# Optimization experiments

Measured on AMD Instinct MI355X. Metric: run time of the kernel, lower is better.

Reference implementation:

```python
import jax, jax.numpy as jnp
import numpy as np

EPS = 1e-6

def _rms_norm(x, w):
    # normalize over last dim (head_dim)
    var = jnp.mean(jnp.square(x), axis=-1, keepdims=True)
    return x * jax.lax.rsqrt(var + EPS) * w

def _rotate_half(x):
    half = x.shape[-1] // 2
    first, second = x[..., :half], x[..., half:]
    return jnp.concatenate([-second, first], axis=-1)

def _apply_rope(x, cos, sin):
    # x: [B,H,S,D]; cos/sin: [B,S,D] -> broadcast over heads
    return x * cos[:, None] + _rotate_half(x) * sin[:, None]

def setup_inputs() -> dict:
    key = jax.random.key(0)
    ks = jax.random.split(key, 10)
    B, Sq, Sk, Dm, H = 2, 2048, 2048, 2048, 16
    hd = Dm // H
    scale = 1.0 / np.sqrt(Dm)
    return {
        "x": jax.random.normal(ks[0], (B, Sq, Dm), jnp.float32),
        "context": jax.random.normal(ks[1], (B, Sk, Dm), jnp.float32),
        "cos_q": jax.random.uniform(ks[2], (B, Sq, hd), jnp.float32),
        "sin_q": jax.random.uniform(ks[3], (B, Sq, hd), jnp.float32),
        "cos_k": jax.random.uniform(ks[4], (B, Sk, hd), jnp.float32),
        "sin_k": jax.random.uniform(ks[5], (B, Sk, hd), jnp.float32),
        "Wq": jax.random.normal(ks[6], (Dm, Dm), jnp.float32) * scale,
        "Wk": jax.random.normal(ks[7], (Dm, Dm), jnp.float32) * scale,
        "Wv": jax.random.normal(ks[8], (Dm, Dm), jnp.float32) * scale,
        "Wo": jax.random.normal(ks[9], (Dm, Dm), jnp.float32) * scale,
        "q_norm_w": jnp.ones((hd,), jnp.float32),
        "k_norm_w": jnp.ones((hd,), jnp.float32),
    }

def reference(x, context, cos_q, sin_q, cos_k, sin_k, Wq, Wk, Wv, Wo, q_norm_w, k_norm_w):
    B, Sq, Dm = x.shape
    hd = q_norm_w.shape[0]
    H = Dm // hd
    # projections (torch Linear: y = x @ W.T), reshape to [B,H,S,D]
    q = (x @ Wq.T).reshape(B, Sq, H, hd).transpose(0, 2, 1, 3)
    k = (context @ Wk.T).reshape(B, -1, H, hd).transpose(0, 2, 1, 3)
    v = (context @ Wv.T).reshape(B, -1, H, hd).transpose(0, 2, 1, 3)
    # per-head QK RMSNorm
    q = _rms_norm(q, q_norm_w)
    k = _rms_norm(k, k_norm_w)
    # RoPE
    q = _apply_rope(q, cos_q, sin_q)
    k = _apply_rope(k, cos_k, sin_k)
    # SDPA, scale = 1/sqrt(head_dim)
    scale = 1.0 / np.sqrt(hd).astype(np.float32)
    scores = jnp.einsum('bhqd,bhkd->bhqk', q, k) * scale
    attn = jax.nn.softmax(scores, axis=-1)
    y = jnp.einsum('bhqk,bhkd->bhqd', attn, v)
    y = y.transpose(0, 2, 1, 3).reshape(B, Sq, Dm)
    return y @ Wo.T
```

## Files before the change

### kernel.cpp

```cpp
#include <hip/hip_runtime.h>


typedef __attribute__((ext_vector_type(8))) short bf16x8;
typedef __attribute__((ext_vector_type(4))) float f32x4;

#define AS1(p) ((__attribute__((address_space(1))) void*)(p))
#define AS3(p) ((__attribute__((address_space(3))) void*)(p))

__device__ __forceinline__ unsigned short f2bf(float f) {
  unsigned int u = __float_as_uint(f);
  u += 0x7fffu + ((u >> 16) & 1u);
  return (unsigned short)(u >> 16);
}

constexpr int B_ = 2, S_ = 2048, DM = 2048, H_ = 16, HD = 128;
constexpr int M_ = B_ * S_;

__global__ __launch_bounds__(256) void castbf(const float* __restrict__ X,
                                              unsigned short* __restrict__ Y, int n4) {
  int i = blockIdx.x * 256 + threadIdx.x;
  if (i >= n4) return;
  float4 v = ((const float4*)X)[i];
  ushort4 u;
  u.x = f2bf(v.x); u.y = f2bf(v.y); u.z = f2bf(v.z); u.w = f2bf(v.w);
  ((ushort4*)Y)[i] = u;
}

__global__ __launch_bounds__(256) void gemm_bt(const unsigned short* __restrict__ A,
                                               const unsigned short* __restrict__ Bw,
                                               float* __restrict__ C,
                                               int M, int N, int K) {
  __shared__ unsigned short lA[128 * 32];
  __shared__ unsigned short lB[128 * 32];
  const int tid = threadIdx.x, wave = tid >> 6, lane = tid & 63;
  const int quad = lane >> 4, l16 = lane & 15;
  const int m0 = blockIdx.x * 128, n0 = blockIdx.y * 128;
  const int wm = (wave >> 1) * 64, wn = (wave & 1) * 64;
  f32x4 acc[4][4];
#pragma unroll
  for (int i = 0; i < 4; i++)
#pragma unroll
    for (int j = 0; j < 4; j++) acc[i][j] = (f32x4){0.f, 0.f, 0.f, 0.f};

  for (int k0 = 0; k0 < K; k0 += 32) {
    __syncthreads();
#pragma unroll
    for (int call = 0; call < 2; ++call) {
      int c = wave * 128 + call * 64 + lane;
      int row = c >> 2, s = c & 3;
      int dc = s ^ ((row >> 1) & 3);
      __builtin_amdgcn_global_load_lds(AS1(A + (size_t)(m0 + row) * K + k0 + dc * 8),
                                       AS3(lA + (wave * 128 + call * 64) * 8), 16, 0, 0);
      __builtin_amdgcn_global_load_lds(AS1(Bw + (size_t)(n0 + row) * K + k0 + dc * 8),
                                       AS3(lB + (wave * 128 + call * 64) * 8), 16, 0, 0);
    }
    __syncthreads();

    bf16x8 af[4], bfr[4];
#pragma unroll
    for (int i = 0; i < 4; i++) {
      int r = wm + i * 16 + l16;
      af[i] = *(const bf16x8*)(lA + r * 32 + (quad ^ ((r >> 1) & 3)) * 8);
      int cN = wn + i * 16 + l16;
      bfr[i] = *(const bf16x8*)(lB + cN * 32 + (quad ^ ((cN >> 1) & 3)) * 8);
    }
#pragma unroll
    for (int i = 0; i < 4; i++)
#pragma unroll
      for (int j = 0; j < 4; j++)
        acc[i][j] = __builtin_amdgcn_mfma_f32_16x16x32_bf16(af[i], bfr[j], acc[i][j], 0, 0, 0);
  }
#pragma unroll
  for (int i = 0; i < 4; i++)
#pragma unroll
    for (int j = 0; j < 4; j++) {
      float* cp = C + (size_t)(m0 + wm + i * 16 + quad * 4) * N + (n0 + wn + j * 16 + l16);
#pragma unroll
      for (int r = 0; r < 4; r++) cp[(size_t)r * N] = acc[i][j][r];
    }
}

__global__ __launch_bounds__(256) void normrope(const float* __restrict__ X,
                                                const float* __restrict__ Cs,
                                                const float* __restrict__ Sn,
                                                const float* __restrict__ W,
                                                unsigned short* __restrict__ Out,
                                                float scale) {
  int gw = (blockIdx.x * 256 + threadIdx.x) >> 6;
  int lane = threadIdx.x & 63;
  int h = gw & 15, bs = gw >> 4;
  int s = bs & (S_ - 1), b = bs >> 11;
  const float* xr = X + (size_t)gw * HD;
  float x0 = xr[lane], x1 = xr[lane + 64];
  float ss = x0 * x0 + x1 * x1;
#pragma unroll
  for (int off = 32; off > 0; off >>= 1) ss += __shfl_xor(ss, off);
  float rr = rsqrtf(ss * (1.0f / 128.0f) + 1e-6f);
  float n0 = x0 * rr * W[lane], n1 = x1 * rr * W[lane + 64];
  const float* cp = Cs + (size_t)bs * HD;
  const float* sp = Sn + (size_t)bs * HD;
  float o0 = (n0 * cp[lane] - n1 * sp[lane]) * scale;
  float o1 = (n1 * cp[lane + 64] + n0 * sp[lane + 64]) * scale;
  unsigned short* orow = Out + (((size_t)(b * H_ + h)) * S_ + s) * HD;
  orow[lane] = f2bf(o0);
  orow[lane + 64] = f2bf(o1);
}

__global__ __launch_bounds__(256) void vtrans(const float* __restrict__ Vf,
                                              unsigned short* __restrict__ Vt) {
  __shared__ unsigned short tile[128 * 72];
  const int tid = threadIdx.x;
  const int sc = blockIdx.x & 31;
  const int bh = blockIdx.x >> 5;
  const int b = bh >> 4, h = bh & 15;
  const int s0 = sc * 64;
#pragma unroll
  for (int it = 0; it < 8; ++it) {
    int ci = it * 256 + tid;
    int s = ci >> 5, dq = ci & 31;
    float4 v = *(const float4*)(Vf + ((size_t)(b * S_ + s0 + s)) * DM + h * HD + dq * 4);
    unsigned short* tp = tile + (dq * 4) * 72 + s;
    tp[0] = f2bf(v.x); tp[72] = f2bf(v.y); tp[144] = f2bf(v.z); tp[216] = f2bf(v.w);
  }
  __syncthreads();
#pragma unroll
  for (int it = 0; it < 4; ++it) {
    int cj = it * 256 + tid;
    int d = cj >> 3, scx = cj & 7;
    bf16x8 vv = *(const bf16x8*)(tile + d * 72 + scx * 8);
    *(bf16x8*)(Vt + ((size_t)bh * HD + d) * S_ + s0 + scx * 8) = vv;
  }
}

__global__ __launch_bounds__(256) void flash(const unsigned short* __restrict__ Q,
                                             const unsigned short* __restrict__ Kt,
                                             const unsigned short* __restrict__ Vt,
                                             unsigned short* __restrict__ Y) {
  __shared__ unsigned short lK[32 * HD];
  __shared__ unsigned short lV[HD * 32];
  __shared__ unsigned short lP[4 * 32 * 32];
  const int tid = threadIdx.x, wave = tid >> 6, lane = tid & 63;
  const int quad = lane >> 4, l16 = lane & 15;
  const int qb = blockIdx.x & 15;
  const int bh = blockIdx.x >> 4;
  const int b = bh >> 4, h = bh & 15;
  const int q0 = qb * 128 + wave * 32;

  bf16x8 aq[2][4];
#pragma unroll
  for (int u = 0; u < 2; u++) {
    const unsigned short* qrow = Q + ((size_t)bh * S_ + q0 + u * 16 + l16) * HD;
#pragma unroll
    for (int t = 0; t < 4; t++) aq[u][t] = *(const bf16x8*)(qrow + t * 32 + quad * 8);
  }
  f32x4 o[2][8];
#pragma unroll
  for (int u = 0; u < 2; u++)
#pragma unroll
    for (int t = 0; t < 8; t++) o[u][t] = (f32x4){0.f, 0.f, 0.f, 0.f};
  float lsum[2][4] = {{0.f, 0.f, 0.f, 0.f}, {0.f, 0.f, 0.f, 0.f}};

  const unsigned short* kbase = Kt + (size_t)bh * S_ * HD;
  const unsigned short* vbase = Vt + (size_t)bh * HD * S_;
  unsigned short* lPw = lP + wave * 1024;
  const int mrow = quad * 4;
  const int xsl = (l16 >> 1) & 3;

  for (int k0 = 0; k0 < S_; k0 += 32) {
    __syncthreads();
#pragma unroll
    for (int call = 0; call < 2; ++call) {
      int c = wave * 128 + call * 64 + lane;
      int key = c >> 4, sk = c & 15;
      int dck = sk ^ (key & 15);
      __builtin_amdgcn_global_load_lds(AS1(kbase + (size_t)(k0 + key) * HD + dck * 8),
                                       AS3(lK + (wave * 128 + call * 64) * 8), 16, 0, 0);
      int dv = c >> 2, sv = c & 3;
      int kc = sv ^ ((dv >> 1) & 3);
      __builtin_amdgcn_global_load_lds(AS1(vbase + (size_t)dv * S_ + k0 + kc * 8),
                                       AS3(lV + (wave * 128 + call * 64) * 8), 16, 0, 0);
    }
    __syncthreads();

    f32x4 s0[2] = {(f32x4){0.f, 0.f, 0.f, 0.f}, (f32x4){0.f, 0.f, 0.f, 0.f}};
    f32x4 s1[2] = {(f32x4){0.f, 0.f, 0.f, 0.f}, (f32x4){0.f, 0.f, 0.f, 0.f}};
    {
      const unsigned short* krow0 = lK + l16 * HD;
      const unsigned short* krow1 = lK + (16 + l16) * HD;
#pragma unroll
      for (int t = 0; t < 4; t++) {
        int dcq = t * 4 + quad;
        bf16x8 kf0 = *(const bf16x8*)(krow0 + (dcq ^ l16) * 8);
        bf16x8 kf1 = *(const bf16x8*)(krow1 + (dcq ^ l16) * 8);
#pragma unroll
        for (int u = 0; u < 2; u++) {
          s0[u] = __builtin_amdgcn_mfma_f32_16x16x32_bf16(aq[u][t], kf0, s0[u], 0, 0, 0);
          s1[u] = __builtin_amdgcn_mfma_f32_16x16x32_bf16(aq[u][t], kf1, s1[u], 0, 0, 0);
        }
      }
    }
#pragma unroll
    for (int u = 0; u < 2; u++) {
      unsigned short* lPu = lPw + u * 512;
#pragma unroll
      for (int r = 0; r < 4; r++) {
        int m = mrow + r;
        int sx = (m >> 1) & 3;
        float p0 = __expf(s0[u][r]);
        float p1 = __expf(s1[u][r]);
        lsum[u][r] += p0 + p1;
        int kc0 = l16 >> 3;
        lPu[m * 32 + ((kc0 ^ sx)) * 8 + (l16 & 7)] = f2bf(p0);
        lPu[m * 32 + (((kc0 + 2) ^ sx)) * 8 + (l16 & 7)] = f2bf(p1);
      }
    }
    bf16x8 pf[2];
#pragma unroll
    for (int u = 0; u < 2; u++)
      pf[u] = *(const bf16x8*)(lPw + u * 512 + l16 * 32 + (quad ^ xsl) * 8);
#pragma unroll
    for (int t = 0; t < 8; t++) {
      bf16x8 vf = *(const bf16x8*)(lV + (t * 16 + l16) * 32 + (quad ^ xsl) * 8);
#pragma unroll
      for (int u = 0; u < 2; u++)
        o[u][t] = __builtin_amdgcn_mfma_f32_16x16x32_bf16(pf[u], vf, o[u][t], 0, 0, 0);
    }
  }

#pragma unroll
  for (int off = 1; off < 16; off <<= 1) {
#pragma unroll
    for (int u = 0; u < 2; u++)
#pragma unroll
      for (int r = 0; r < 4; r++) lsum[u][r] += __shfl_xor(lsum[u][r], off);
  }
  float inv[2][4];
#pragma unroll
  for (int u = 0; u < 2; u++)
#pragma unroll
    for (int r = 0; r < 4; r++) inv[u][r] = 1.0f / lsum[u][r];
#pragma unroll
  for (int u = 0; u < 2; u++)
#pragma unroll
    for (int t = 0; t < 8; t++)
#pragma unroll
      for (int r = 0; r < 4; r++) {
        size_t idx = ((size_t)b * S_ + q0 + u * 16 + mrow + r) * DM + h * HD + t * 16 + l16;
        Y[idx] = f2bf(o[u][t][r] * inv[u][r]);
      }
}

extern "C" void kernel_launch(void* const* d_in, const int* in_sizes, int n_in,
                              void* d_out, int out_size, void* d_ws, size_t ws_size,
                              hipStream_t stream) {
  const float* x    = (const float*)d_in[0];
  const float* ctx  = (const float*)d_in[1];
  const float* cosq = (const float*)d_in[2];
  const float* sinq = (const float*)d_in[3];
  const float* cosk = (const float*)d_in[4];
  const float* sink = (const float*)d_in[5];
  const float* Wq   = (const float*)d_in[6];
  const float* Wk   = (const float*)d_in[7];
  const float* Wv   = (const float*)d_in[8];
  const float* Wo   = (const float*)d_in[9];
  const float* qw   = (const float*)d_in[10];
  const float* kw   = (const float*)d_in[11];

  char* ws = (char*)d_ws;
  const size_t ACT2 = (size_t)M_ * DM * 2;
  const size_t W2   = (size_t)DM * DM * 2;
  unsigned short* xb  = (unsigned short*)(ws);
  unsigned short* cb  = (unsigned short*)(ws + ACT2);
  unsigned short* Wqb = (unsigned short*)(ws + 2 * ACT2);
  unsigned short* Wkb = (unsigned short*)(ws + 2 * ACT2 + W2);
  unsigned short* Wvb = (unsigned short*)(ws + 2 * ACT2 + 2 * W2);
  unsigned short* Wob = (unsigned short*)(ws + 2 * ACT2 + 3 * W2);
  float*          Pf  = (float*)(ws + 2 * ACT2 + 4 * W2);
  unsigned short* qn = xb;
  unsigned short* kn = Wqb;
  unsigned short* vt = cb;
  unsigned short* yb = (unsigned short*)Pf;

  const float scale = 0.0883883476483184f;
  dim3 gg(M_ / 128, DM / 128);

  castbf<<<M_ * DM / 1024, 256, 0, stream>>>(x, xb, M_ * DM / 4);
  castbf<<<M_ * DM / 1024, 256, 0, stream>>>(ctx, cb, M_ * DM / 4);
  castbf<<<DM * DM / 1024, 256, 0, stream>>>(Wq, Wqb, DM * DM / 4);
  castbf<<<DM * DM / 1024, 256, 0, stream>>>(Wk, Wkb, DM * DM / 4);
  castbf<<<DM * DM / 1024, 256, 0, stream>>>(Wv, Wvb, DM * DM / 4);
  castbf<<<DM * DM / 1024, 256, 0, stream>>>(Wo, Wob, DM * DM / 4);

  gemm_bt<<<gg, 256, 0, stream>>>(xb, Wqb, Pf, M_, DM, DM);
  normrope<<<M_ * H_ / 4, 256, 0, stream>>>(Pf, cosq, sinq, qw, qn, scale);

  gemm_bt<<<gg, 256, 0, stream>>>(cb, Wkb, Pf, M_, DM, DM);
  normrope<<<M_ * H_ / 4, 256, 0, stream>>>(Pf, cosk, sink, kw, kn, 1.0f);

  gemm_bt<<<gg, 256, 0, stream>>>(cb, Wvb, Pf, M_, DM, DM);
  vtrans<<<B_ * H_ * (S_ / 64), 256, 0, stream>>>(Pf, vt);

  flash<<<B_ * H_ * (S_ / 128), 256, 0, stream>>>(qn, kn, vt, yb);

  gemm_bt<<<gg, 256, 0, stream>>>(yb, Wob, (float*)d_out, M_, DM, DM);

  (void)in_sizes; (void)n_in; (void)out_size; (void)ws_size;
}
```

Baseline: 561.6 us.

## Batch QKV GEMMs into one launch with bf16 outputs; retile flash attention

The three projection GEMMs become a single launch with grid z selecting Q, K or V, and they write bf16 instead of fp32. That halves the intermediate traffic and removes the launch serialization between them. normrope and vtrans now read bf16 inputs. The flash kernel moves to 128-thread blocks covering 64 queries, with 64-key K/V tiles per sync, so there are twice as many blocks and half as many barriers per key. Rounding the projections to bf16 before the RMSNorm adds precision loss. The workspace now needs room for three separate projection buffers.

New measurement: 496.1 us. -11.7%, faster.

```diff
diff --git a/kernel.cpp b/kernel.cpp
--- a/kernel.cpp
+++ b/kernel.cpp
@@ -11,6 +11,9 @@
   unsigned int u = __float_as_uint(f);
   u += 0x7fffu + ((u >> 16) & 1u);
   return (unsigned short)(u >> 16);
+}
+__device__ __forceinline__ float bf2f(unsigned short u) {
+  return __uint_as_float(((unsigned int)u) << 16);
 }
 
 constexpr int B_ = 2, S_ = 2048, DM = 2048, H_ = 16, HD = 128;
@@ -24,6 +27,68 @@
   ushort4 u;
   u.x = f2bf(v.x); u.y = f2bf(v.y); u.z = f2bf(v.z); u.w = f2bf(v.w);
   ((ushort4*)Y)[i] = u;
+}
+
+__global__ __launch_bounds__(256) void gemm_qkv(const unsigned short* __restrict__ xb,
+                                                const unsigned short* __restrict__ cb,
+                                                const unsigned short* __restrict__ Wq,
+                                                const unsigned short* __restrict__ Wk,
+                                                const unsigned short* __restrict__ Wv,
+                                                unsigned short* __restrict__ Pq,
+                                                unsigned short* __restrict__ Pk,
+                                                unsigned short* __restrict__ Pv) {
+  __shared__ unsigned short lA[128 * 32];
+  __shared__ unsigned short lB[128 * 32];
+  const int z = blockIdx.z;
+  const unsigned short* A  = (z == 0) ? xb : cb;
+  const unsigned short* Bw = (z == 0) ? Wq : (z == 1) ? Wk : Wv;
+  unsigned short* C        = (z == 0) ? Pq : (z == 1) ? Pk : Pv;
+  const int tid = threadIdx.x, wave = tid >> 6, lane = tid & 63;
+  const int quad = lane >> 4, l16 = lane & 15;
+  const int m0 = blockIdx.x * 128, n0 = blockIdx.y * 128;
+  const int wm = (wave >> 1) * 64, wn = (wave & 1) * 64;
+  f32x4 acc[4][4];
+#pragma unroll
+  for (int i = 0; i < 4; i++)
+#pragma unroll
+    for (int j = 0; j < 4; j++) acc[i][j] = (f32x4){0.f, 0.f, 0.f, 0.f};
+
+  for (int k0 = 0; k0 < DM; k0 += 32) {
+    __syncthreads();
+#pragma unroll
+    for (int call = 0; call < 2; ++call) {
+      int c = wave * 128 + call * 64 + lane;
+      int row = c >> 2, s = c & 3;
+      int dc = s ^ ((row >> 1) & 3);
+      __builtin_amdgcn_global_load_lds(AS1(A + (size_t)(m0 + row) * DM + k0 + dc * 8),
+                                       AS3(lA + (wave * 128 + call * 64) * 8), 16, 0, 0);
+      __builtin_amdgcn_global_load_lds(AS1(Bw + (size_t)(n0 + row) * DM + k0 + dc * 8),
+                                       AS3(lB + (wave * 128 + call * 64) * 8), 16, 0, 0);
+    }
+    __syncthreads();
+
+    bf16x8 af[4], bfr[4];
+#pragma unroll
+    for (int i = 0; i < 4; i++) {
+      int r = wm + i * 16 + l16;
+      af[i] = *(const bf16x8*)(lA + r * 32 + (quad ^ ((r >> 1) & 3)) * 8);
+      int cN = wn + i * 16 + l16;
+      bfr[i] = *(const bf16x8*)(lB + cN * 32 + (quad ^ ((cN >> 1) & 3)) * 8);
+    }
+#pragma unroll
+    for (int i = 0; i < 4; i++)
+#pragma unroll
+      for (int j = 0; j < 4; j++)
+        acc[i][j] = __builtin_amdgcn_mfma_f32_16x16x32_bf16(af[i], bfr[j], acc[i][j], 0, 0, 0);
+  }
+#pragma unroll
+  for (int i = 0; i < 4; i++)
+#pragma unroll
+    for (int j = 0; j < 4; j++) {
+      unsigned short* cp = C + (size_t)(m0 + wm + i * 16 + quad * 4) * DM + (n0 + wn + j * 16 + l16);
+#pragma unroll
+      for (int r = 0; r < 4; r++) cp[(size_t)r * DM] = f2bf(acc[i][j][r]);
+    }
 }
 
 __global__ __launch_bounds__(256) void gemm_bt(const unsigned short* __restrict__ A,
@@ -80,7 +145,7 @@
     }
 }
 
-__global__ __launch_bounds__(256) void normrope(const float* __restrict__ X,
+__global__ __launch_bounds__(256) void normrope(const unsigned short* __restrict__ X,
                                                 const float* __restrict__ Cs,
                                                 const float* __restrict__ Sn,
                                                 const float* __restrict__ W,
@@ -90,8 +155,8 @@
   int lane = threadIdx.x & 63;
   int h = gw & 15, bs = gw >> 4;
   int s = bs & (S_ - 1), b = bs >> 11;
-  const float* xr = X + (size_t)gw * HD;
-  float x0 = xr[lane], x1 = xr[lane + 64];
+  const unsigned short* xr = X + (size_t)gw * HD;
+  float x0 = bf2f(xr[lane]), x1 = bf2f(xr[lane + 64]);
   float ss = x0 * x0 + x1 * x1;
 #pragma unroll
   for (int off = 32; off > 0; off >>= 1) ss += __shfl_xor(ss, off);
@@ -106,7 +171,7 @@
   orow[lane + 64] = f2bf(o1);
 }
 
-__global__ __launch_bounds__(256) void vtrans(const float* __restrict__ Vf,
+__global__ __launch_bounds__(256) void vtrans(const unsigned short* __restrict__ Vf,
                                               unsigned short* __restrict__ Vt) {
   __shared__ unsigned short tile[128 * 72];
   const int tid = threadIdx.x;
@@ -115,12 +180,13 @@
   const int b = bh >> 4, h = bh & 15;
   const int s0 = sc * 64;
 #pragma unroll
-  for (int it = 0; it < 8; ++it) {
+  for (int it = 0; it < 4; ++it) {
     int ci = it * 256 + tid;
-    int s = ci >> 5, dq = ci & 31;
-    float4 v = *(const float4*)(Vf + ((size_t)(b * S_ + s0 + s)) * DM + h * HD + dq * 4);
-    unsigned short* tp = tile + (dq * 4) * 72 + s;
-    tp[0] = f2bf(v.x); tp[72] = f2bf(v.y); tp[144] = f2bf(v.z); tp[216] = f2bf(v.w);
+    int s = ci >> 4, dc = ci & 15;
+    bf16x8 v = *(const bf16x8*)(Vf + ((size_t)(b * S_ + s0 + s)) * DM + h * HD + dc * 8);
+    unsigned short* tp = tile + (dc * 8) * 72 + s;
+#pragma unroll
+    for (int e = 0; e < 8; e++) tp[e * 72] = (unsigned short)v[e];
   }
   __syncthreads();
 #pragma unroll
@@ -132,19 +198,19 @@
   }
 }
 
-__global__ __launch_bounds__(256) void flash(const unsigned short* __restrict__ Q,
+__global__ __launch_bounds__(128) void flash(const unsigned short* __restrict__ Q,
                                              const unsigned short* __restrict__ Kt,
                                              const unsigned short* __restrict__ Vt,
                                              unsigned short* __restrict__ Y) {
-  __shared__ unsigned short lK[32 * HD];
-  __shared__ unsigned short lV[HD * 32];
-  __shared__ unsigned short lP[4 * 32 * 32];
+  __shared__ unsigned short lK[64 * HD];
+  __shared__ unsigned short lV[HD * 64];
+  __shared__ unsigned short lP[2 * 1024];
   const int tid = threadIdx.x, wave = tid >> 6, lane = tid & 63;
   const int quad = lane >> 4, l16 = lane & 15;
-  const int qb = blockIdx.x & 15;
-  const int bh = blockIdx.x >> 4;
+  const int qb = blockIdx.x & 31;
+  const int bh = blockIdx.x >> 5;
   const int b = bh >> 4, h = bh & 15;
-  const int q0 = qb * 128 + wave * 32;
+  const int q0 = qb * 64 + wave * 32;
 
   bf16x8 aq[2][4];
 #pragma unroll
@@ -165,65 +231,69 @@
   unsigned short* lPw = lP + wave * 1024;
   const int mrow = quad * 4;
   const int xsl = (l16 >> 1) & 3;
-
-  for (int k0 = 0; k0 < S_; k0 += 32) {
-    __syncthreads();
-#pragma unroll
-    for (int call = 0; call < 2; ++call) {
-      int c = wave * 128 + call * 64 + lane;
+  const int xsl7 = (l16 >> 1) & 7;
+
+  for (int k0 = 0; k0 < S_; k0 += 64) {
+    __syncthreads();
+#pragma unroll
+    for (int call = 0; call < 8; ++call) {
+      int c = call * 128 + wave * 64 + lane;
       int key = c >> 4, sk = c & 15;
       int dck = sk ^ (key & 15);
       __builtin_amdgcn_global_load_lds(AS1(kbase + (size_t)(k0 + key) * HD + dck * 8),
-                                       AS3(lK + (wave * 128 + call * 64) * 8), 16, 0, 0);
-      int dv = c >> 2, sv = c & 3;
-      int kc = sv ^ ((dv >> 1) & 3);
+                                       AS3(lK + (call * 128 + wave * 64) * 8), 16, 0, 0);
+      int dv = c >> 3, sv = c & 7;
+      int kc = sv ^ ((dv >> 1) & 7);
       __builtin_amdgcn_global_load_lds(AS1(vbase + (size_t)dv * S_ + k0 + kc * 8),
-                                       AS3(lV + (wave * 128 + call * 64) * 8), 16, 0, 0);
-    }
-    __syncthreads();
-
-    f32x4 s0[2] = {(f32x4){0.f, 0.f, 0.f, 0.f}, (f32x4){0.f, 0.f, 0.f, 0.f}};
-    f32x4 s1[2] = {(f32x4){0.f, 0.f, 0.f, 0.f}, (f32x4){0.f, 0.f, 0.f, 0.f}};
-    {
-      const unsigned short* krow0 = lK + l16 * HD;
-      const unsigned short* krow1 = lK + (16 + l16) * HD;
-#pragma unroll
-      for (int t = 0; t < 4; t++) {
-        int dcq = t * 4 + quad;
-        bf16x8 kf0 = *(const bf16x8*)(krow0 + (dcq ^ l16) * 8);
-        bf16x8 kf1 = *(const bf16x8*)(krow1 + (dcq ^ l16) * 8);
-#pragma unroll
-        for (int u = 0; u < 2; u++) {
-          s0[u] = __builtin_amdgcn_mfma_f32_16x16x32_bf16(aq[u][t], kf0, s0[u], 0, 0, 0);
-          s1[u] = __builtin_amdgcn_mfma_f32_16x16x32_bf16(aq[u][t], kf1, s1[u], 0, 0, 0);
+                                       AS3(lV + (call * 128 + wave * 64) * 8), 16, 0, 0);
+    }
+    __syncthreads();
+
+#pragma unroll
+    for (int h2 = 0; h2 < 2; ++h2) {
+      f32x4 s0[2] = {(f32x4){0.f, 0.f, 0.f, 0.f}, (f32x4){0.f, 0.f, 0.f, 0.f}};
+      f32x4 s1[2] = {(f32x4){0.f, 0.f, 0.f, 0.f}, (f32x4){0.f, 0.f, 0.f, 0.f}};
+      {
+        const unsigned short* krow0 = lK + (h2 * 32 + l16) * HD;
+        const unsigned short* krow1 = krow0 + 16 * HD;
+#pragma unroll
+        for (int t = 0; t < 4; t++) {
+          int dcq = t * 4 + quad;
+          bf16x8 kf0 = *(const bf16x8*)(krow0 + (dcq ^ l16) * 8);
+          bf16x8 kf1 = *(const bf16x8*)(krow1 + (dcq ^ l16) * 8);
+#pragma unroll
+          for (int u = 0; u < 2; u++) {
+            s0[u] = __builtin_amdgcn_mfma_f32_16x16x32_bf16(aq[u][t], kf0, s0[u], 0, 0, 0);
+            s1[u] = __builtin_amdgcn_mfma_f32_16x16x32_bf16(aq[u][t], kf1, s1[u], 0, 0, 0);
+          }
         }
       }
-    }
-#pragma unroll
-    for (int u = 0; u < 2; u++) {
-      unsigned short* lPu = lPw + u * 512;
-#pragma unroll
-      for (int r = 0; r < 4; r++) {
-        int m = mrow + r;
-        int sx = (m >> 1) & 3;
-        float p0 = __expf(s0[u][r]);
-        float p1 = __expf(s1[u][r]);
-        lsum[u][r] += p0 + p1;
-        int kc0 = l16 >> 3;
-        lPu[m * 32 + ((kc0 ^ sx)) * 8 + (l16 & 7)] = f2bf(p0);
-        lPu[m * 32 + (((kc0 + 2) ^ sx)) * 8 + (l16 & 7)] = f2bf(p1);
+#pragma unroll
+      for (int u = 0; u < 2; u++) {
+        unsigned short* lPu = lPw + u * 512;
+#pragma unroll
+        for (int r = 0; r < 4; r++) {
+          int m = mrow + r;
+          int sx = (m >> 1) & 3;
+          float p0 = __expf(s0[u][r]);
+          float p1 = __expf(s1[u][r]);
+          lsum[u][r] += p0 + p1;
+          int kc0 = l16 >> 3;
+          lPu[m * 32 + ((kc0 ^ sx)) * 8 + (l16 & 7)] = f2bf(p0);
+          lPu[m * 32 + (((kc0 + 2) ^ sx)) * 8 + (l16 & 7)] = f2bf(p1);
+        }
       }
-    }
-    bf16x8 pf[2];
-#pragma unroll
-    for (int u = 0; u < 2; u++)
-      pf[u] = *(const bf16x8*)(lPw + u * 512 + l16 * 32 + (quad ^ xsl) * 8);
-#pragma unroll
-    for (int t = 0; t < 8; t++) {
-      bf16x8 vf = *(const bf16x8*)(lV + (t * 16 + l16) * 32 + (quad ^ xsl) * 8);
+      bf16x8 pf[2];
 #pragma unroll
       for (int u = 0; u < 2; u++)
-        o[u][t] = __builtin_amdgcn_mfma_f32_16x16x32_bf16(pf[u], vf, o[u][t], 0, 0, 0);
+        pf[u] = *(const bf16x8*)(lPw + u * 512 + l16 * 32 + (quad ^ xsl) * 8);
+#pragma unroll
+      for (int t = 0; t < 8; t++) {
+        bf16x8 vf = *(const bf16x8*)(lV + (t * 16 + l16) * 64 + ((h2 * 4 + quad) ^ xsl7) * 8);
+#pragma unroll
+        for (int u = 0; u < 2; u++)
+          o[u][t] = __builtin_amdgcn_mfma_f32_16x16x32_bf16(pf[u], vf, o[u][t], 0, 0, 0);
+      }
     }
   }
 
@@ -275,14 +345,15 @@
   unsigned short* Wkb = (unsigned short*)(ws + 2 * ACT2 + W2);
   unsigned short* Wvb = (unsigned short*)(ws + 2 * ACT2 + 2 * W2);
   unsigned short* Wob = (unsigned short*)(ws + 2 * ACT2 + 3 * W2);
-  float*          Pf  = (float*)(ws + 2 * ACT2 + 4 * W2);
+  unsigned short* Pq  = (unsigned short*)(ws + 2 * ACT2 + 4 * W2);
+  unsigned short* Pk  = (unsigned short*)(ws + 3 * ACT2 + 4 * W2);
+  unsigned short* Pv  = (unsigned short*)(ws + 4 * ACT2 + 4 * W2);
   unsigned short* qn = xb;
   unsigned short* kn = Wqb;
   unsigned short* vt = cb;
-  unsigned short* yb = (unsigned short*)Pf;
+  unsigned short* yb = Pq;
 
   const float scale = 0.0883883476483184f;
-  dim3 gg(M_ / 128, DM / 128);
 
   castbf<<<M_ * DM / 1024, 256, 0, stream>>>(x, xb, M_ * DM / 4);
   castbf<<<M_ * DM / 1024, 256, 0, stream>>>(ctx, cb, M_ * DM / 4);
@@ -291,17 +362,16 @@
   castbf<<<DM * DM / 1024, 256, 0, stream>>>(Wv, Wvb, DM * DM / 4);
   castbf<<<DM * DM / 1024, 256, 0, stream>>>(Wo, Wob, DM * DM / 4);
 
-  gemm_bt<<<gg, 256, 0, stream>>>(xb, Wqb, Pf, M_, DM, DM);
-  normrope<<<M_ * H_ / 4, 256, 0, stream>>>(Pf, cosq, sinq, qw, qn, scale);
-
-  gemm_bt<<<gg, 256, 0, stream>>>(cb, Wkb, Pf, M_, DM, DM);
-  normrope<<<M_ * H_ / 4, 256, 0, stream>>>(Pf, cosk, sink, kw, kn, 1.0f);
-
-  gemm_bt<<<gg, 256, 0, stream>>>(cb, Wvb, Pf, M_, DM, DM);
-  vtrans<<<B_ * H_ * (S_ / 64), 256, 0, stream>>>(Pf, vt);
-
-  flash<<<B_ * H_ * (S_ / 128), 256, 0, stream>>>(qn, kn, vt, yb);
-
+  dim3 gq(M_ / 128, DM / 128, 3);
+  gemm_qkv<<<gq, 256, 0, stream>>>(xb, cb, Wqb, Wkb, Wvb, Pq, Pk, Pv);
+
+  normrope<<<M_ * H_ / 4, 256, 0, stream>>>(Pq, cosq, sinq, qw, qn, scale);
+  normrope<<<M_ * H_ / 4, 256, 0, stream>>>(Pk, cosk, sink, kw, kn, 1.0f);
+  vtrans<<<B_ * H_ * (S_ / 64), 256, 0, stream>>>(Pv, vt);
+
+  flash<<<B_ * H_ * (S_ / 64), 128, 0, stream>>>(qn, kn, vt, yb);
+
+  dim3 gg(M_ / 128, DM / 128);
   gemm_bt<<<gg, 256, 0, stream>>>(yb, Wob, (float*)d_out, M_, DM, DM);
 
   (void)in_sizes; (void)n_in; (void)out_size; (void)ws_size;
```
